# Performance work log

Measured on AMD Instinct MI355X. Metric: run time of the kernel, lower is better.

## Reference

```python
import jax, jax.numpy as jnp
import numpy as np
import math

B, T, C = 1, 2048, 512
NH, NKV, HD, W = 8, 4, 64, 128  # heads, kv heads, head_dim, window_size
THETA = 10000.0
EPS = 1e-6


def _rms(x, w):
    # RMSNorm over last (head_dim) axis with learnable scale w
    return x * jax.lax.rsqrt(jnp.mean(x * x, axis=-1, keepdims=True) + EPS) * w


def _rope(x, cos, sin):
    # x: (B, H, T, HD); cos/sin: (T, HD//2). Half-split rotation.
    h = x.shape[-1] // 2
    x1, x2 = x[..., :h], x[..., h:]
    return jnp.concatenate([x1 * cos - x2 * sin, x2 * cos + x1 * sin], axis=-1)


def setup_inputs():
    key = jax.random.key(0)
    ks = jax.random.split(key, 5)
    x = jax.random.normal(ks[0], (B, T, C), jnp.float32)
    s = 1.0 / math.sqrt(C)
    W_q = jax.random.normal(ks[1], (C, NH * HD), jnp.float32) * s
    W_k = jax.random.normal(ks[2], (C, NKV * HD), jnp.float32) * s
    W_v = jax.random.normal(ks[3], (C, NKV * HD), jnp.float32) * s
    W_o = jax.random.normal(ks[4], (C, C), jnp.float32) * s
    q_norm_w = jnp.ones((HD,), jnp.float32)
    k_norm_w = jnp.ones((HD,), jnp.float32)
    pos = jnp.arange(T, dtype=jnp.float32)
    inv_freq = 1.0 / (THETA ** (jnp.arange(0, HD, 2, dtype=jnp.float32) / HD))
    ang = pos[:, None] * inv_freq[None, :]  # (T, HD//2)
    return {"x": x, "W_q": W_q, "W_k": W_k, "W_v": W_v, "W_o": W_o,
            "q_norm_w": q_norm_w, "k_norm_w": k_norm_w,
            "cos": jnp.cos(ang), "sin": jnp.sin(ang)}


def reference(x, W_q, W_k, W_v, W_o, q_norm_w, k_norm_w, cos, sin):
    q = (x @ W_q).reshape(B, T, NH, HD).transpose(0, 2, 1, 3)   # (B,NH,T,HD)
    k = (x @ W_k).reshape(B, T, NKV, HD).transpose(0, 2, 1, 3)  # (B,NKV,T,HD)
    v = (x @ W_v).reshape(B, T, NKV, HD).transpose(0, 2, 1, 3)
    q = _rope(q, cos, sin)
    k = _rope(k, cos, sin)
    q = _rms(q, q_norm_w)
    k = _rms(k, k_norm_w)
    g = NH // NKV  # GQA group size
    k = jnp.repeat(k, g, axis=1)  # (B,NH,T,HD)
    v = jnp.repeat(v, g, axis=1)
    # causal sliding-window: gather W-length windows ending at each position
    kp = jnp.pad(k, ((0, 0), (0, 0), (W - 1, 0), (0, 0)))
    vp = jnp.pad(v, ((0, 0), (0, 0), (W - 1, 0), (0, 0)))
    idx = jnp.arange(T)[:, None] + jnp.arange(W)[None, :]  # (T, W)
    kw = kp[:, :, idx, :]  # (B,NH,T,W,HD)
    vw = vp[:, :, idx, :]
    valid = jnp.arange(W)[None, :] >= (W - 1 - jnp.arange(T))[:, None]  # (T,W)
    attn = jnp.einsum('bhtd,bhtwd->bhtw', q, kw) / math.sqrt(HD)
    attn = jnp.where(valid[None, None], attn, -jnp.inf)
    attn = jax.nn.softmax(attn, axis=-1)
    out = jnp.einsum('bhtw,bhtwd->bhtd', attn, vw)  # (B,NH,T,HD)
    out = out.transpose(0, 2, 1, 3).reshape(B, T, C)
    return out @ W_o
```

## Files before the change

### kernel.cpp

```cpp
#include <hip/hip_runtime.h>
#include <hip/hip_bf16.h>
#include <math.h>

typedef float  f32x4  __attribute__((ext_vector_type(4)));
typedef short  s16x4  __attribute__((ext_vector_type(4)));
typedef short  s16x8  __attribute__((ext_vector_type(8)));
typedef unsigned short u16;

__device__ inline u16 f2b(float f) {
    __hip_bfloat16 h = __float2bfloat16(f);
    return *reinterpret_cast<u16*>(&h);
}

__global__ __launch_bounds__(256) void prep(const float* __restrict__ x,
    const float* __restrict__ Wq, const float* __restrict__ Wk,
    const float* __restrict__ Wv, const float* __restrict__ Wo,
    u16* __restrict__ xb, u16* __restrict__ Wt, u16* __restrict__ Wot)
{
    const int tid = threadIdx.x, bid = blockIdx.x;
    if (bid >= 192) {
        int i = ((bid - 192) * 256 + tid) * 8;
        float4 v0 = *(const float4*)(x + i);
        float4 v1 = *(const float4*)(x + i + 4);
        ushort4 o0 = { f2b(v0.x), f2b(v0.y), f2b(v0.z), f2b(v0.w) };
        ushort4 o1 = { f2b(v1.x), f2b(v1.y), f2b(v1.z), f2b(v1.w) };
        *(ushort4*)(xb + i)     = o0;
        *(ushort4*)(xb + i + 4) = o1;
        return;
    }
    __shared__ u16 Tsh[64][72];
    const float* src; u16* dst; int N, base, kt, nt;
    if (bid < 64)       { src = Wq; dst = Wt;  N = 512; base = 0;   kt = bid >> 3;       nt = bid & 7; }
    else if (bid < 96)  { src = Wk; dst = Wt;  N = 256; base = 512; kt = (bid-64) >> 2;  nt = (bid-64) & 3; }
    else if (bid < 128) { src = Wv; dst = Wt;  N = 256; base = 768; kt = (bid-96) >> 2;  nt = (bid-96) & 3; }
    else                { src = Wo; dst = Wot; N = 512; base = 0;   kt = (bid-128) >> 3; nt = (bid-128) & 7; }
    const int k0 = kt * 64, n0 = nt * 64;
    const int r = tid >> 2, c0 = (tid & 3) * 16;
#pragma unroll
    for (int j = 0; j < 4; ++j) {
        float4 v = *(const float4*)(src + (size_t)(k0 + r) * N + n0 + c0 + j * 4);
        Tsh[c0 + j*4 + 0][r] = f2b(v.x);
        Tsh[c0 + j*4 + 1][r] = f2b(v.y);
        Tsh[c0 + j*4 + 2][r] = f2b(v.z);
        Tsh[c0 + j*4 + 3][r] = f2b(v.w);
    }
    __syncthreads();
    const int n = tid >> 2, kc = (tid & 3) * 16;
    u16* op = dst + (size_t)(base + n0 + n) * 512 + k0 + kc;
    *(s16x8*)(op)     = *(const s16x8*)&Tsh[n][kc];
    *(s16x8*)(op + 8) = *(const s16x8*)&Tsh[n][kc + 8];
}

__global__ __launch_bounds__(256) void gemm_mfma(const u16* __restrict__ A,
    const u16* __restrict__ Bt, float* __restrict__ C, int ldc)
{
    __shared__ u16 Ash[64][72];
    __shared__ u16 Bsh[64][72];
    const int tid = threadIdx.x;
    const int m0b = blockIdx.y * 64, n0b = blockIdx.x * 64;
    const int lane = tid & 63, wv = tid >> 6;
    const int q = lane & 15, g = lane >> 4;
    const int wm = (wv & 1) * 32, wn = (wv >> 1) * 32;
    const int sr = tid >> 2, sc = (tid & 3) * 16;
    f32x4 acc[2][2] = {{{0,0,0,0},{0,0,0,0}},{{0,0,0,0},{0,0,0,0}}};
    for (int k0 = 0; k0 < 512; k0 += 64) {
        s16x8 a0 = *(const s16x8*)(A  + (size_t)(m0b + sr) * 512 + k0 + sc);
        s16x8 a1 = *(const s16x8*)(A  + (size_t)(m0b + sr) * 512 + k0 + sc + 8);
        s16x8 b0 = *(const s16x8*)(Bt + (size_t)(n0b + sr) * 512 + k0 + sc);
        s16x8 b1 = *(const s16x8*)(Bt + (size_t)(n0b + sr) * 512 + k0 + sc + 8);
        __syncthreads();
        *(s16x8*)&Ash[sr][sc]     = a0;
        *(s16x8*)&Ash[sr][sc + 8] = a1;
        *(s16x8*)&Bsh[sr][sc]     = b0;
        *(s16x8*)&Bsh[sr][sc + 8] = b1;
        __syncthreads();
#pragma unroll
        for (int kk = 0; kk < 64; kk += 32) {
            s16x8 af0 = *(const s16x8*)&Ash[wm + q][kk + g*8];
            s16x8 af1 = *(const s16x8*)&Ash[wm + 16 + q][kk + g*8];
            s16x8 bf0 = *(const s16x8*)&Bsh[wn + q][kk + g*8];
            s16x8 bf1 = *(const s16x8*)&Bsh[wn + 16 + q][kk + g*8];
            acc[0][0] = __builtin_amdgcn_mfma_f32_16x16x32_bf16(af0, bf0, acc[0][0], 0, 0, 0);
            acc[0][1] = __builtin_amdgcn_mfma_f32_16x16x32_bf16(af0, bf1, acc[0][1], 0, 0, 0);
            acc[1][0] = __builtin_amdgcn_mfma_f32_16x16x32_bf16(af1, bf0, acc[1][0], 0, 0, 0);
            acc[1][1] = __builtin_amdgcn_mfma_f32_16x16x32_bf16(af1, bf1, acc[1][1], 0, 0, 0);
        }
    }
#pragma unroll
    for (int mt = 0; mt < 2; ++mt)
#pragma unroll
        for (int nt = 0; nt < 2; ++nt)
#pragma unroll
            for (int r = 0; r < 4; ++r)
                C[(size_t)(m0b + wm + mt*16 + g*4 + r) * ldc + n0b + wn + nt*16 + q] = acc[mt][nt][r];
}

__global__ __launch_bounds__(256) void rope_rms_b(const float* __restrict__ qkv,
    const float* __restrict__ cosT, const float* __restrict__ sinT,
    const float* __restrict__ qw, const float* __restrict__ kw,
    u16* __restrict__ qnb, u16* __restrict__ knb, u16* __restrict__ vb)
{
    const int lane = threadIdx.x & 63;
    const int gid  = blockIdx.x * 4 + (threadIdx.x >> 6);
    const int t = gid >> 4, hh = gid & 15;
    if (hh >= 12) {
        int vh = hh - 12;
        vb[(size_t)t * 256 + vh * 64 + lane] =
            f2b(qkv[(size_t)t * 1024 + 768 + vh * 64 + lane]);
        return;
    }
    const float* src; u16* dst; const float* nw;
    if (hh < 8) { src = qkv + (size_t)t*1024 + hh*64;           dst = qnb + (size_t)t*512 + hh*64;     nw = qw; }
    else        { src = qkv + (size_t)t*1024 + 512 + (hh-8)*64; dst = knb + (size_t)t*256 + (hh-8)*64; nw = kw; }
    float y = src[lane];
    float o = __shfl(y, lane ^ 32);
    float c = cosT[t * 32 + (lane & 31)];
    float s = sinT[t * 32 + (lane & 31)];
    float r = (lane < 32) ? (y * c - o * s) : (y * c + o * s);
    float ss = r * r;
#pragma unroll
    for (int off = 32; off; off >>= 1) ss += __shfl_xor(ss, off);
    dst[lane] = f2b(r * rsqrtf(ss * (1.0f/64.0f) + 1e-6f) * nw[lane]);
}

__global__ __launch_bounds__(256) void swa_mfma(const u16* __restrict__ qnb,
    const u16* __restrict__ knb, const u16* __restrict__ vb,
    u16* __restrict__ attb)
{
    __shared__ u16 Ksh[192][72];
    __shared__ u16 Vt[64][202];
    const int tid = threadIdx.x;
    const int h = blockIdx.y, kvh = h >> 1;
    const int t0 = blockIdx.x * 64;
    for (int i = 0; i < 6; ++i) {
        int idx = i * 256 + tid;
        int j = idx >> 3, d0 = (idx & 7) * 8;
        int kt = t0 - 127 + j;
        s16x8 val = {0,0,0,0,0,0,0,0};
        if (kt >= 0) val = *(const s16x8*)(knb + (size_t)kt * 256 + kvh * 64 + d0);
        *(s16x8*)&Ksh[j][d0] = val;
    }
    for (int cch = 0; cch < 6; ++cch) {
        int w  = cch * 32 + (tid & 31);
        int d0 = (tid >> 5) * 8;
        int kt = t0 - 127 + w;
        s16x8 val = {0,0,0,0,0,0,0,0};
        if (kt >= 0) val = *(const s16x8*)(vb + (size_t)kt * 256 + kvh * 64 + d0);
#pragma unroll
        for (int jj = 0; jj < 8; ++jj) Vt[d0 + jj][w] = ((const u16*)&val)[jj];
    }
    __syncthreads();
    const int wv = tid >> 6, lane = tid & 63;
    const int q = lane & 15, g = lane >> 4;
    const int tw = t0 + wv * 16;
    const int t = tw + q;
    const u16* qp = qnb + (size_t)t * 512 + h * 64;
    s16x8 qf0 = *(const s16x8*)(qp + g * 8);
    s16x8 qf1 = *(const s16x8*)(qp + 32 + g * 8);
    float s[9][4];
    float mx = -INFINITY;
    for (int wt = 0; wt < 9; ++wt) {
        int ldsrow = wv * 16 + wt * 16 + q;
        s16x8 kf0 = *(const s16x8*)&Ksh[ldsrow][g * 8];
        s16x8 kf1 = *(const s16x8*)&Ksh[ldsrow][32 + g * 8];
        f32x4 accv = {0, 0, 0, 0};
        accv = __builtin_amdgcn_mfma_f32_16x16x32_bf16(kf0, qf0, accv, 0, 0, 0);
        accv = __builtin_amdgcn_mfma_f32_16x16x32_bf16(kf1, qf1, accv, 0, 0, 0);
#pragma unroll
        for (int r = 0; r < 4; ++r) {
            int woff = wt * 16 + g * 4 + r;
            int key  = tw - 127 + woff;
            bool ok = (woff >= q) && (woff <= q + 127) && (key >= 0);
            float sv = ok ? accv[r] * 0.125f : -INFINITY;
            s[wt][r] = sv;
            mx = fmaxf(mx, sv);
        }
    }
    mx = fmaxf(mx, __shfl_xor(mx, 16));
    mx = fmaxf(mx, __shfl_xor(mx, 32));
    float sum = 0.f;
    s16x4 pb[9];
    for (int wt = 0; wt < 9; ++wt) {
#pragma unroll
        for (int r = 0; r < 4; ++r) {
            float p = __expf(s[wt][r] - mx);
            sum += p;
            pb[wt][r] = (short)f2b(p);
        }
    }
    sum += __shfl_xor(sum, 16);
    sum += __shfl_xor(sum, 32);
    float inv = 1.0f / sum;
    f32x4 oacc[4];
#pragma unroll
    for (int dt = 0; dt < 4; ++dt) {
        f32x4 a = {0, 0, 0, 0};
        for (int wt = 0; wt < 9; ++wt) {
            int col = wv * 16 + wt * 16 + g * 4;
            s16x4 vf = *(const s16x4*)&Vt[dt * 16 + q][col];
            a = __builtin_amdgcn_mfma_f32_16x16x16bf16_1k(vf, pb[wt], a, 0, 0, 0);
        }
        oacc[dt] = a;
    }
    __syncthreads();
    float (*Osh)[16][68] = (float (*)[16][68])&Ksh[0][0];
#pragma unroll
    for (int dt = 0; dt < 4; ++dt)
#pragma unroll
        for (int r = 0; r < 4; ++r)
            Osh[wv][q][dt * 16 + g * 4 + r] = oacc[dt][r] * inv;
    __syncthreads();
    const int qq = lane >> 2, dd0 = (lane & 3) * 16;
    u16* op = attb + (size_t)(tw + qq) * 512 + h * 64 + dd0;
#pragma unroll
    for (int jj = 0; jj < 4; ++jj) {
        float4 vvv = *(const float4*)&Osh[wv][qq][dd0 + jj * 4];
        ushort4 ov = { f2b(vvv.x), f2b(vvv.y), f2b(vvv.z), f2b(vvv.w) };
        *(ushort4*)(op + jj * 4) = ov;
    }
}

extern "C" void kernel_launch(void* const* d_in, const int* in_sizes, int n_in,
                              void* d_out, int out_size, void* d_ws, size_t ws_size,
                              hipStream_t stream)
{
    const float* x    = (const float*)d_in[0];
    const float* Wq   = (const float*)d_in[1];
    const float* Wk   = (const float*)d_in[2];
    const float* Wv   = (const float*)d_in[3];
    const float* Wo   = (const float*)d_in[4];
    const float* qw   = (const float*)d_in[5];
    const float* kw   = (const float*)d_in[6];
    const float* cosT = (const float*)d_in[7];
    const float* sinT = (const float*)d_in[8];

    u16* ws   = (u16*)d_ws;
    u16* xb   = ws;
    u16* Wt   = xb  + (size_t)2048 * 512;
    u16* Wot  = Wt  + (size_t)1024 * 512;
    float* qkv = (float*)(Wot + (size_t)512 * 512);
    u16* qnb  = (u16*)(qkv + (size_t)2048 * 1024);
    u16* knb  = qnb + (size_t)2048 * 512;
    u16* vb   = knb + (size_t)2048 * 256;
    u16* attb = vb  + (size_t)2048 * 256;

    dim3 blk(256);
    hipLaunchKernelGGL(prep, dim3(704), blk, 0, stream, x, Wq, Wk, Wv, Wo, xb, Wt, Wot);
    hipLaunchKernelGGL(gemm_mfma, dim3(16, 32), blk, 0, stream, xb, Wt, qkv, 1024);
    hipLaunchKernelGGL(rope_rms_b, dim3(8192), blk, 0, stream,
                       qkv, cosT, sinT, qw, kw, qnb, knb, vb);
    hipLaunchKernelGGL(swa_mfma, dim3(32, 8), blk, 0, stream, qnb, knb, vb, attb);
    hipLaunchKernelGGL(gemm_mfma, dim3(8, 32), blk, 0, stream, attb, Wot, (float*)d_out, 512);
}
```

Baseline: 39.69 us.

## Fuse RoPE and RMSNorm into attention kernel and emit bf16 QKV from GEMM

```diff
diff --git a/kernel.cpp b/kernel.cpp
--- a/kernel.cpp
+++ b/kernel.cpp
@@ -11,6 +11,11 @@
     __hip_bfloat16 h = __float2bfloat16(f);
     return *reinterpret_cast<u16*>(&h);
 }
+__device__ inline float b2f(u16 v) {
+    return __uint_as_float(((unsigned)v) << 16);
+}
+__device__ inline void st_out(float* p, float v) { *p = v; }
+__device__ inline void st_out(u16* p, float v)   { *p = f2b(v); }
 
 __global__ __launch_bounds__(256) void prep(const float* __restrict__ x,
     const float* __restrict__ Wq, const float* __restrict__ Wk,
@@ -51,8 +56,9 @@
     *(s16x8*)(op + 8) = *(const s16x8*)&Tsh[n][kc + 8];
 }
 
+template<typename OutT>
 __global__ __launch_bounds__(256) void gemm_mfma(const u16* __restrict__ A,
-    const u16* __restrict__ Bt, float* __restrict__ C, int ldc)
+    const u16* __restrict__ Bt, OutT* __restrict__ C, int ldc)
 {
     __shared__ u16 Ash[64][72];
     __shared__ u16 Bsh[64][72];
@@ -92,39 +98,13 @@
         for (int nt = 0; nt < 2; ++nt)
 #pragma unroll
             for (int r = 0; r < 4; ++r)
-                C[(size_t)(m0b + wm + mt*16 + g*4 + r) * ldc + n0b + wn + nt*16 + q] = acc[mt][nt][r];
-}
-
-__global__ __launch_bounds__(256) void rope_rms_b(const float* __restrict__ qkv,
+                st_out(&C[(size_t)(m0b + wm + mt*16 + g*4 + r) * ldc + n0b + wn + nt*16 + q],
+                       acc[mt][nt][r]);
+}
+
+__global__ __launch_bounds__(256) void swa_mfma(const u16* __restrict__ qkvb,
     const float* __restrict__ cosT, const float* __restrict__ sinT,
     const float* __restrict__ qw, const float* __restrict__ kw,
-    u16* __restrict__ qnb, u16* __restrict__ knb, u16* __restrict__ vb)
-{
-    const int lane = threadIdx.x & 63;
-    const int gid  = blockIdx.x * 4 + (threadIdx.x >> 6);
-    const int t = gid >> 4, hh = gid & 15;
-    if (hh >= 12) {
-        int vh = hh - 12;
-        vb[(size_t)t * 256 + vh * 64 + lane] =
-            f2b(qkv[(size_t)t * 1024 + 768 + vh * 64 + lane]);
-        return;
-    }
-    const float* src; u16* dst; const float* nw;
-    if (hh < 8) { src = qkv + (size_t)t*1024 + hh*64;           dst = qnb + (size_t)t*512 + hh*64;     nw = qw; }
-    else        { src = qkv + (size_t)t*1024 + 512 + (hh-8)*64; dst = knb + (size_t)t*256 + (hh-8)*64; nw = kw; }
-    float y = src[lane];
-    float o = __shfl(y, lane ^ 32);
-    float c = cosT[t * 32 + (lane & 31)];
-    float s = sinT[t * 32 + (lane & 31)];
-    float r = (lane < 32) ? (y * c - o * s) : (y * c + o * s);
-    float ss = r * r;
-#pragma unroll
-    for (int off = 32; off; off >>= 1) ss += __shfl_xor(ss, off);
-    dst[lane] = f2b(r * rsqrtf(ss * (1.0f/64.0f) + 1e-6f) * nw[lane]);
-}
-
-__global__ __launch_bounds__(256) void swa_mfma(const u16* __restrict__ qnb,
-    const u16* __restrict__ knb, const u16* __restrict__ vb,
     u16* __restrict__ attb)
 {
     __shared__ u16 Ksh[192][72];
@@ -134,29 +114,90 @@
     const int t0 = blockIdx.x * 64;
     for (int i = 0; i < 6; ++i) {
         int idx = i * 256 + tid;
-        int j = idx >> 3, d0 = (idx & 7) * 8;
+        int j = idx >> 3, e = idx & 7, d0 = e * 8;
         int kt = t0 - 127 + j;
-        s16x8 val = {0,0,0,0,0,0,0,0};
-        if (kt >= 0) val = *(const s16x8*)(knb + (size_t)kt * 256 + kvh * 64 + d0);
-        *(s16x8*)&Ksh[j][d0] = val;
+        if (kt < 0) {
+            s16x8 z = {0,0,0,0,0,0,0,0};
+            *(s16x8*)&Ksh[j][d0] = z;
+        } else {
+            s16x8 raw = *(const s16x8*)(qkvb + (size_t)kt * 1024 + 512 + kvh * 64 + d0);
+            float kv[8], ov[8];
+#pragma unroll
+            for (int ii = 0; ii < 8; ++ii) kv[ii] = b2f((u16)raw[ii]);
+#pragma unroll
+            for (int ii = 0; ii < 8; ++ii) ov[ii] = __shfl_xor(kv[ii], 4);
+            const float* cp = cosT + kt * 32 + (e & 3) * 8;
+            const float* sp = sinT + kt * 32 + (e & 3) * 8;
+            float4 c0 = *(const float4*)(cp),     c1 = *(const float4*)(cp + 4);
+            float4 s0 = *(const float4*)(sp),     s1 = *(const float4*)(sp + 4);
+            float cf[8] = {c0.x,c0.y,c0.z,c0.w,c1.x,c1.y,c1.z,c1.w};
+            float sf[8] = {s0.x,s0.y,s0.z,s0.w,s1.x,s1.y,s1.z,s1.w};
+            const bool lo = (e < 4);
+            float r[8]; float ssl = 0.f;
+#pragma unroll
+            for (int ii = 0; ii < 8; ++ii) {
+                r[ii] = lo ? (kv[ii]*cf[ii] - ov[ii]*sf[ii])
+                           : (kv[ii]*cf[ii] + ov[ii]*sf[ii]);
+                ssl += r[ii] * r[ii];
+            }
+            ssl += __shfl_xor(ssl, 1);
+            ssl += __shfl_xor(ssl, 2);
+            ssl += __shfl_xor(ssl, 4);
+            float scale = rsqrtf(ssl * (1.0f / 64.0f) + 1e-6f);
+            float4 w0 = *(const float4*)(kw + d0), w1 = *(const float4*)(kw + d0 + 4);
+            float wf[8] = {w0.x,w0.y,w0.z,w0.w,w1.x,w1.y,w1.z,w1.w};
+            s16x8 outv;
+#pragma unroll
+            for (int ii = 0; ii < 8; ++ii) outv[ii] = (short)f2b(r[ii] * scale * wf[ii]);
+            *(s16x8*)&Ksh[j][d0] = outv;
+        }
     }
     for (int cch = 0; cch < 6; ++cch) {
         int w  = cch * 32 + (tid & 31);
         int d0 = (tid >> 5) * 8;
         int kt = t0 - 127 + w;
         s16x8 val = {0,0,0,0,0,0,0,0};
-        if (kt >= 0) val = *(const s16x8*)(vb + (size_t)kt * 256 + kvh * 64 + d0);
+        if (kt >= 0) val = *(const s16x8*)(qkvb + (size_t)kt * 1024 + 768 + kvh * 64 + d0);
 #pragma unroll
         for (int jj = 0; jj < 8; ++jj) Vt[d0 + jj][w] = ((const u16*)&val)[jj];
     }
-    __syncthreads();
     const int wv = tid >> 6, lane = tid & 63;
     const int q = lane & 15, g = lane >> 4;
     const int tw = t0 + wv * 16;
     const int t = tw + q;
-    const u16* qp = qnb + (size_t)t * 512 + h * 64;
-    s16x8 qf0 = *(const s16x8*)(qp + g * 8);
-    s16x8 qf1 = *(const s16x8*)(qp + 32 + g * 8);
+    s16x8 qf0, qf1;
+    {
+        const u16* qp = qkvb + (size_t)t * 1024 + h * 64;
+        s16x8 q0r = *(const s16x8*)(qp + g * 8);
+        s16x8 q1r = *(const s16x8*)(qp + 32 + g * 8);
+        const float* cp = cosT + t * 32 + g * 8;
+        const float* sp = sinT + t * 32 + g * 8;
+        float4 c0 = *(const float4*)(cp), c1 = *(const float4*)(cp + 4);
+        float4 s0 = *(const float4*)(sp), s1 = *(const float4*)(sp + 4);
+        float cf[8] = {c0.x,c0.y,c0.z,c0.w,c1.x,c1.y,c1.z,c1.w};
+        float sf[8] = {s0.x,s0.y,s0.z,s0.w,s1.x,s1.y,s1.z,s1.w};
+        float rl[8], rh[8]; float ssl = 0.f;
+#pragma unroll
+        for (int ii = 0; ii < 8; ++ii) {
+            float ql = b2f((u16)q0r[ii]), qh = b2f((u16)q1r[ii]);
+            rl[ii] = ql * cf[ii] - qh * sf[ii];
+            rh[ii] = qh * cf[ii] + ql * sf[ii];
+            ssl += rl[ii]*rl[ii] + rh[ii]*rh[ii];
+        }
+        ssl += __shfl_xor(ssl, 16);
+        ssl += __shfl_xor(ssl, 32);
+        float scale = rsqrtf(ssl * (1.0f / 64.0f) + 1e-6f);
+        float4 wl0 = *(const float4*)(qw + g * 8), wl1 = *(const float4*)(qw + g * 8 + 4);
+        float4 wh0 = *(const float4*)(qw + 32 + g * 8), wh1 = *(const float4*)(qw + 32 + g * 8 + 4);
+        float wlo[8] = {wl0.x,wl0.y,wl0.z,wl0.w,wl1.x,wl1.y,wl1.z,wl1.w};
+        float whi[8] = {wh0.x,wh0.y,wh0.z,wh0.w,wh1.x,wh1.y,wh1.z,wh1.w};
+#pragma unroll
+        for (int ii = 0; ii < 8; ++ii) {
+            qf0[ii] = (short)f2b(rl[ii] * scale * wlo[ii]);
+            qf1[ii] = (short)f2b(rh[ii] * scale * whi[ii]);
+        }
+    }
+    __syncthreads();
     float s[9][4];
     float mx = -INFINITY;
     for (int wt = 0; wt < 9; ++wt) {
@@ -236,19 +277,16 @@
 
     u16* ws   = (u16*)d_ws;
     u16* xb   = ws;
-    u16* Wt   = xb  + (size_t)2048 * 512;
-    u16* Wot  = Wt  + (size_t)1024 * 512;
-    float* qkv = (float*)(Wot + (size_t)512 * 512);
-    u16* qnb  = (u16*)(qkv + (size_t)2048 * 1024);
-    u16* knb  = qnb + (size_t)2048 * 512;
-    u16* vb   = knb + (size_t)2048 * 256;
-    u16* attb = vb  + (size_t)2048 * 256;
+    u16* Wt   = xb   + (size_t)2048 * 512;
+    u16* Wot  = Wt   + (size_t)1024 * 512;
+    u16* qkvb = Wot  + (size_t)512 * 512;
+    u16* attb = qkvb + (size_t)2048 * 1024;
 
     dim3 blk(256);
     hipLaunchKernelGGL(prep, dim3(704), blk, 0, stream, x, Wq, Wk, Wv, Wo, xb, Wt, Wot);
-    hipLaunchKernelGGL(gemm_mfma, dim3(16, 32), blk, 0, stream, xb, Wt, qkv, 1024);
-    hipLaunchKernelGGL(rope_rms_b, dim3(8192), blk, 0, stream,
-                       qkv, cosT, sinT, qw, kw, qnb, knb, vb);
-    hipLaunchKernelGGL(swa_mfma, dim3(32, 8), blk, 0, stream, qnb, knb, vb, attb);
-    hipLaunchKernelGGL(gemm_mfma, dim3(8, 32), blk, 0, stream, attb, Wot, (float*)d_out, 512);
-}
+    hipLaunchKernelGGL((gemm_mfma<u16>), dim3(16, 32), blk, 0, stream, xb, Wt, qkvb, 1024);
+    hipLaunchKernelGGL(swa_mfma, dim3(32, 8), blk, 0, stream,
+                       qkvb, cosT, sinT, qw, kw, attb);
+    hipLaunchKernelGGL((gemm_mfma<float>), dim3(8, 32), blk, 0, stream,
+                       attb, Wot, (float*)d_out, 512);
+}
```

Result: faster. 35.47 us (-10.6%).
